# Optimization experiments

Measured on AMD Instinct MI355X. Metric: run time of the kernel, lower is better.

The kernel has to match this reference:

```python
import jax, jax.numpy as jnp
import numpy as np

LB_WEIGHT = 0.01  # load_balance_loss_weight


def setup_inputs() -> dict:
    key = jax.random.key(0)
    ks = jax.random.split(key, 5)
    B, S, D, F, E = 2, 2048, 1024, 4096, 8
    scale = 0.02
    return {
        "x": jax.random.normal(ks[0], (B, S, D), dtype=jnp.float32),
        "Wr": jax.random.normal(ks[1], (E, D), dtype=jnp.float32) * scale,
        "W1": jax.random.normal(ks[2], (E, F, D), dtype=jnp.float32) * scale,
        "b1": jnp.zeros((E, F), dtype=jnp.float32),
        "W2": jax.random.normal(ks[3], (E, D, F), dtype=jnp.float32) * scale,
        "b2": jnp.zeros((E, D), dtype=jnp.float32),
        "top_k": 2,
    }


def reference(x, Wr, W1, b1, W2, b2, top_k):
    B, S, D = x.shape
    E = Wr.shape[0]
    x_flat = x.reshape(-1, D)                      # (T, D)

    # Router: softmax over experts, then top-k with renormalized gates.
    router_logits = x_flat @ Wr.T                  # (T, E)
    router_probs = jax.nn.softmax(router_logits, axis=-1)
    topk_p, topk_idx = jax.lax.top_k(router_probs, top_k)   # (T, K)
    topk_p = topk_p / jnp.sum(topk_p, axis=-1, keepdims=True)

    # Combine weights per expert: w[t, e] = sum_k topk_p[t, k] * [idx[t, k] == e]
    one_hot = jax.nn.one_hot(topk_idx, E, dtype=x.dtype)     # (T, K, E)
    combine = jnp.einsum("tk,tke->te", topk_p, one_hot)      # (T, E)

    # Expert FFNs (dense over all experts; masked-out experts get zero weight).
    # FeedForward: Linear(D->F) -> GELU -> Linear(F->D); dropout is identity (eval).
    h = jnp.einsum("td,efd->tef", x_flat, W1) + b1           # (T, E, F)
    h = jax.nn.gelu(h)
    expert_out = jnp.einsum("tef,edf->ted", h, W2) + b2      # (T, E, D)

    out_flat = jnp.einsum("te,ted->td", combine, expert_out) # (T, D)
    output = out_flat.reshape(B, S, D)

    # Load-balance aux loss.
    expert_usage = jnp.mean(router_probs, axis=0)            # (E,)
    aux_loss = LB_WEIGHT * jnp.sum((expert_usage - 1.0 / E) ** 2)
    return output, aux_loss
```

## Files before the change

kernel.cpp:

```cpp
#include <hip/hip_runtime.h>
#include <hip/hip_bf16.h>
#include <stdint.h>

#define D_DIM 1024
#define F_DIM 4096
#define E_NUM 8
#define BM2 256
#define BN2 128
#define BK 64
#define MAXTILES 80
#define MAXT256 40

typedef __attribute__((ext_vector_type(4))) float f32x4;
typedef __attribute__((ext_vector_type(8))) short bf16x8;

#define C_CNT   0
#define C_CUR   8
#define C_OFF   16
#define C_NT    25
#define C_TE    26
#define C_TR    (26+MAXTILES)
#define C_USAGE (26+2*MAXTILES)

__device__ __forceinline__ void gload_lds16(const void* g, void* l) {
  __builtin_amdgcn_global_load_lds((const __attribute__((address_space(1))) void*)g,
                                   (__attribute__((address_space(3))) void*)l, 16, 0, 0);
}

__device__ __forceinline__ float bf2f(unsigned short u) {
  union { unsigned int i; float f; } c; c.i = ((unsigned int)u) << 16; return c.f;
}

__global__ void cvt_k(const float* __restrict__ s, unsigned short* __restrict__ d, int n4) {
  const int stride = gridDim.x * blockDim.x;
  for (int i = blockIdx.x * blockDim.x + threadIdx.x; i < n4; i += stride) {
    float4 v = ((const float4*)s)[i];
    __hip_bfloat16 h0 = __float2bfloat16(v.x);
    __hip_bfloat16 h1 = __float2bfloat16(v.y);
    __hip_bfloat16 h2 = __float2bfloat16(v.z);
    __hip_bfloat16 h3 = __float2bfloat16(v.w);
    ushort4 o;
    o.x = *(unsigned short*)&h0; o.y = *(unsigned short*)&h1;
    o.z = *(unsigned short*)&h2; o.w = *(unsigned short*)&h3;
    ((ushort4*)d)[i] = o;
  }
}

__global__ __launch_bounds__(256) void router_k(
    const float* __restrict__ x, const float* __restrict__ Wr,
    int* __restrict__ t2i, float* __restrict__ t2g,
    float* __restrict__ usage_part, unsigned short* __restrict__ xb, int T) {
  __shared__ float us[4][E_NUM];
  const int wave = threadIdx.x >> 6;
  const int lane = threadIdx.x & 63;
  const int gw = blockIdx.x * 4 + wave;
  const float4* xt = (const float4*)(x + (size_t)gw * D_DIM);
  const float4* wr4 = (const float4*)Wr;
  unsigned short* xrow = xb + (size_t)gw * D_DIM;
  float l[E_NUM] = {0.f,0.f,0.f,0.f,0.f,0.f,0.f,0.f};
#pragma unroll
  for (int it = 0; it < D_DIM / 256; it++) {
    const int i4 = it * 64 + lane;
    const float4 xv = xt[i4];
    __hip_bfloat16 c0 = __float2bfloat16(xv.x), c1 = __float2bfloat16(xv.y);
    __hip_bfloat16 c2 = __float2bfloat16(xv.z), c3 = __float2bfloat16(xv.w);
    ushort4 ov; ov.x = *(unsigned short*)&c0; ov.y = *(unsigned short*)&c1;
    ov.z = *(unsigned short*)&c2; ov.w = *(unsigned short*)&c3;
    ((ushort4*)xrow)[i4] = ov;
#pragma unroll
    for (int e = 0; e < E_NUM; e++) {
      const float4 w = wr4[e * (D_DIM / 4) + i4];
      l[e] += xv.x * w.x + xv.y * w.y + xv.z * w.z + xv.w * w.w;
    }
  }
#pragma unroll
  for (int e = 0; e < E_NUM; e++) {
    float v = l[e];
    v += __shfl_xor(v, 32); v += __shfl_xor(v, 16); v += __shfl_xor(v, 8);
    v += __shfl_xor(v, 4);  v += __shfl_xor(v, 2);  v += __shfl_xor(v, 1);
    l[e] = v;
  }
  float m = l[0];
#pragma unroll
  for (int e = 1; e < E_NUM; e++) m = fmaxf(m, l[e]);
  float p[E_NUM]; float s = 0.f;
#pragma unroll
  for (int e = 0; e < E_NUM; e++) { p[e] = expf(l[e] - m); s += p[e]; }
  const float inv = 1.0f / s;
  float v1 = l[0]; int i1 = 0;
#pragma unroll
  for (int e = 1; e < E_NUM; e++) { if (l[e] > v1) { v1 = l[e]; i1 = e; } }
  float v2 = -3.0e38f; int i2 = 0;
#pragma unroll
  for (int e = 0; e < E_NUM; e++) { if (e != i1 && l[e] > v2) { v2 = l[e]; i2 = e; } }
  const float p1 = expf(v1 - m);
  const float p2 = expf(v2 - m);
  const float gd = 1.0f / (p1 + p2);
  if (lane == 0) {
    t2i[gw * 2] = i1; t2i[gw * 2 + 1] = i2;
    t2g[gw * 2] = p1 * gd; t2g[gw * 2 + 1] = p2 * gd;
#pragma unroll
    for (int e = 0; e < E_NUM; e++) us[wave][e] = p[e] * inv;
  }
  __syncthreads();
  if (threadIdx.x < E_NUM) {
    const int e = threadIdx.x;
    usage_part[blockIdx.x * E_NUM + e] = us[0][e] + us[1][e] + us[2][e] + us[3][e];
  }
}

__global__ __launch_bounds__(256) void reduce_k(
    const float* __restrict__ usage_part, const int* __restrict__ t2i,
    int* __restrict__ ctrl, float* __restrict__ aux_out, int nblk, int T2, int T) {
  __shared__ float usum[E_NUM];
  __shared__ int hist[E_NUM];
  if (threadIdx.x < E_NUM) { usum[threadIdx.x] = 0.f; hist[threadIdx.x] = 0; }
  __syncthreads();
  {
    const int e = threadIdx.x & 7;
    const int chunk = threadIdx.x >> 3;
    float s = 0.f;
    for (int i = chunk; i < nblk; i += 32) s += usage_part[i * E_NUM + e];
    atomicAdd(&usum[e], s);
  }
  {
    int h[E_NUM] = {0,0,0,0,0,0,0,0};
    for (int i = threadIdx.x; i < T2; i += 256) h[t2i[i] & 7]++;
#pragma unroll
    for (int e = 0; e < E_NUM; e++) if (h[e]) atomicAdd(&hist[e], h[e]);
  }
  __syncthreads();
  if (threadIdx.x == 0) {
    int off = 0, nt = 0;
    float loss = 0.f;
    for (int e = 0; e < E_NUM; e++) {
      ctrl[C_CNT + e] = hist[e];
      ctrl[C_OFF + e] = off;
      ctrl[C_CUR + e] = off;
      const int c = hist[e];
      const int ntile = (c + BM2 - 1) / BM2;
      for (int i = 0; i < ntile; i++) {
        ctrl[C_TE + nt] = e;
        ctrl[C_TR + nt] = off + i * BM2;
        nt++;
      }
      off += c;
      const float um = usum[e] / (float)T - 1.0f / (float)E_NUM;
      loss += um * um;
    }
    ctrl[C_OFF + E_NUM] = off;
    ctrl[C_NT] = nt;
    aux_out[0] = 0.01f * loss;
  }
}

__global__ void scatter_k(const int* __restrict__ t2i, int* __restrict__ ctrl,
                          int* __restrict__ rmap, int* __restrict__ slots, int T) {
  const int t = blockIdx.x * blockDim.x + threadIdx.x;
  if (t >= T) return;
#pragma unroll
  for (int k = 0; k < 2; k++) {
    const int e = t2i[t * 2 + k];
    const int slot = atomicAdd(&ctrl[C_CUR + e], 1);
    rmap[slot] = t;
    slots[t * 2 + k] = slot;
  }
}

#define STAGE(K0, AL, BL)                                            \
  {                                                                  \
    _Pragma("unroll")                                                \
    for (int i = 0; i < 4; i++) gload_lds16(a_src[i] + (K0), AL[i]); \
    _Pragma("unroll")                                                \
    for (int j = 0; j < 2; j++) gload_lds16(b_src[j] + (K0), BL[j]); \
  }

#define COMPUTE(AC, BC)                                              \
  {                                                                  \
    _Pragma("unroll")                                                \
    for (int kh = 0; kh < 2; ++kh) {                                 \
      const int co = (((kh * 4 + ckq) ^ swz) << 4);                  \
      bf16x8 af[8], bfv[2];                                          \
      _Pragma("unroll")                                              \
      for (int mi = 0; mi < 8; mi++)                                 \
        af[mi] = *(const bf16x8*)((AC) + (rA + mi * 16) * 128 + co); \
      _Pragma("unroll")                                              \
      for (int ni = 0; ni < 2; ni++)                                 \
        bfv[ni] = *(const bf16x8*)((BC) + (rB + ni * 16) * 128 + co);\
      _Pragma("unroll")                                              \
      for (int mi = 0; mi < 8; mi++)                                 \
        _Pragma("unroll")                                            \
        for (int ni = 0; ni < 2; ni++)                               \
          acc[mi][ni] = __builtin_amdgcn_mfma_f32_16x16x32_bf16(af[mi], bfv[ni], acc[mi][ni], 0, 0, 0); \
    }                                                                \
  }

__global__ __launch_bounds__(512, 2) void gemm1_k(
    const unsigned short* __restrict__ xb, const unsigned short* __restrict__ W1b,
    const float* __restrict__ b1, unsigned short* __restrict__ hb,
    const int* __restrict__ rmap, const int* __restrict__ ctrl, int T2) {
  extern __shared__ char smem[];
  const int lin = blockIdx.x;
  const int lin2 = (lin & 7) * 160 + (lin >> 3);
  const int tile = lin2 >> 5;
  const int fbase = (lin2 & 31) * BN2;

  const int nt = ctrl[C_NT];
  if (tile >= nt) return;
  const int e = ctrl[C_TE + tile];
  const int rowbase = ctrl[C_TR + tile];
  const int row_end = ctrl[C_OFF + e + 1];

  const int tid = threadIdx.x;
  const int lane = tid & 63;
  const int wave = tid >> 6;

  const unsigned short* a_src[4];
  const unsigned short* b_src[2];
  char *aL0[4], *aL1[4], *bL0[2], *bL1[2];
#pragma unroll
  for (int i = 0; i < 4; i++) {
    const int c = tid + 512 * i;
    const int r = c >> 3, cc = c & 7;
    const int sc = cc ^ (r & 7);
    int pos = rowbase + r; pos = pos < T2 ? pos : T2 - 1;
    a_src[i] = xb + (size_t)rmap[pos] * D_DIM + sc * 8;
    aL0[i] = smem + c * 16;
    aL1[i] = smem + 32768 + c * 16;
  }
#pragma unroll
  for (int j = 0; j < 2; j++) {
    const int c2 = tid + 512 * j;
    const int r = c2 >> 3, cc = c2 & 7;
    const int sc = cc ^ (r & 7);
    b_src[j] = W1b + ((size_t)e * F_DIM + (size_t)(fbase + r)) * D_DIM + sc * 8;
    bL0[j] = smem + 65536 + c2 * 16;
    bL1[j] = smem + 81920 + c2 * 16;
  }
  const char* As0 = smem;          const char* As1 = smem + 32768;
  const char* Bs0 = smem + 65536;  const char* Bs1 = smem + 81920;

  f32x4 acc[8][2] = {};
  const int wm = wave >> 2, wn = wave & 3;
  const int rA = wm * 128 + (lane & 15);
  const int rB = wn * 32 + (lane & 15);
  const int swz = lane & 7;
  const int ckq = lane >> 4;

  STAGE(0, aL0, bL0);
  const int NK = D_DIM / BK;
  for (int kt = 0; kt < NK; kt += 2) {
    STAGE((kt + 1) * BK, aL1, bL1);
    asm volatile("s_waitcnt vmcnt(6)" ::: "memory");
    __builtin_amdgcn_s_barrier();
    __builtin_amdgcn_sched_barrier(0);
    COMPUTE(As0, Bs0);
    __builtin_amdgcn_sched_barrier(0);
    __builtin_amdgcn_s_barrier();
    if (kt + 2 < NK) {
      STAGE((kt + 2) * BK, aL0, bL0);
      asm volatile("s_waitcnt vmcnt(6)" ::: "memory");
    } else {
      asm volatile("s_waitcnt vmcnt(0)" ::: "memory");
    }
    __builtin_amdgcn_s_barrier();
    __builtin_amdgcn_sched_barrier(0);
    COMPUTE(As1, Bs1);
    __builtin_amdgcn_sched_barrier(0);
    __builtin_amdgcn_s_barrier();
  }

  const int r_rem = row_end - rowbase;
  const float* b1e = b1 + (size_t)e * F_DIM;
  float bias[2];
#pragma unroll
  for (int ni = 0; ni < 2; ni++)
    bias[ni] = b1e[fbase + wn * 32 + ni * 16 + (lane & 15)];
#pragma unroll
  for (int mi = 0; mi < 8; mi++) {
#pragma unroll
    for (int q = 0; q < 4; q++) {
      const int rr = wm * 128 + mi * 16 + (lane >> 4) * 4 + q;
      if (rr < r_rem) {
        unsigned short* hrow = hb + (size_t)(rowbase + rr) * F_DIM;
#pragma unroll
        for (int ni = 0; ni < 2; ni++) {
          const int col = fbase + wn * 32 + ni * 16 + (lane & 15);
          const float v = acc[mi][ni][q] + bias[ni];
          const float u2 = 1.5957691216057308f * (v + 0.044715f * v * v * v);
          const float gg = v / (1.0f + __expf(-u2));
          __hip_bfloat16 hv = __float2bfloat16(gg);
          hrow[col] = *(unsigned short*)&hv;
        }
      }
    }
  }
}

__global__ __launch_bounds__(512, 2) void gemm2_k(
    const unsigned short* __restrict__ hb, const unsigned short* __restrict__ W2b,
    unsigned short* __restrict__ y2, const int* __restrict__ ctrl, int T2) {
  extern __shared__ char smem[];
  const int lin = blockIdx.x;
  const int lin2 = (lin & 7) * 160 + (lin >> 3);
  const int tile = lin2 >> 5;
  const int rest = lin2 & 31;
  const int z = rest >> 3;
  const int dbase = (rest & 7) * BN2;

  const int nt = ctrl[C_NT];
  if (tile >= nt) return;
  const int e = ctrl[C_TE + tile];
  const int rowbase = ctrl[C_TR + tile];
  const int row_end = ctrl[C_OFF + e + 1];
  const int kt0 = z * (F_DIM / BK / 4);

  const int tid = threadIdx.x;
  const int lane = tid & 63;
  const int wave = tid >> 6;

  const unsigned short* a_src[4];
  const unsigned short* b_src[2];
  char *aL0[4], *aL1[4], *bL0[2], *bL1[2];
#pragma unroll
  for (int i = 0; i < 4; i++) {
    const int c = tid + 512 * i;
    const int r = c >> 3, cc = c & 7;
    const int sc = cc ^ (r & 7);
    int pos = rowbase + r; pos = pos < T2 ? pos : T2 - 1;
    a_src[i] = hb + (size_t)pos * F_DIM + sc * 8;
    aL0[i] = smem + c * 16;
    aL1[i] = smem + 32768 + c * 16;
  }
#pragma unroll
  for (int j = 0; j < 2; j++) {
    const int c2 = tid + 512 * j;
    const int r = c2 >> 3, cc = c2 & 7;
    const int sc = cc ^ (r & 7);
    b_src[j] = W2b + ((size_t)e * D_DIM + (size_t)(dbase + r)) * F_DIM + sc * 8;
    bL0[j] = smem + 65536 + c2 * 16;
    bL1[j] = smem + 81920 + c2 * 16;
  }
  const char* As0 = smem;          const char* As1 = smem + 32768;
  const char* Bs0 = smem + 65536;  const char* Bs1 = smem + 81920;

  f32x4 acc[8][2] = {};
  const int wm = wave >> 2, wn = wave & 3;
  const int rA = wm * 128 + (lane & 15);
  const int rB = wn * 32 + (lane & 15);
  const int swz = lane & 7;
  const int ckq = lane >> 4;

  const int NKH = F_DIM / BK / 4;
  STAGE(kt0 * BK, aL0, bL0);
  for (int kt = kt0; kt < kt0 + NKH; kt += 2) {
    STAGE((kt + 1) * BK, aL1, bL1);
    asm volatile("s_waitcnt vmcnt(6)" ::: "memory");
    __builtin_amdgcn_s_barrier();
    __builtin_amdgcn_sched_barrier(0);
    COMPUTE(As0, Bs0);
    __builtin_amdgcn_sched_barrier(0);
    __builtin_amdgcn_s_barrier();
    if (kt + 2 < kt0 + NKH) {
      STAGE((kt + 2) * BK, aL0, bL0);
      asm volatile("s_waitcnt vmcnt(6)" ::: "memory");
    } else {
      asm volatile("s_waitcnt vmcnt(0)" ::: "memory");
    }
    __builtin_amdgcn_s_barrier();
    __builtin_amdgcn_sched_barrier(0);
    COMPUTE(As1, Bs1);
    __builtin_amdgcn_sched_barrier(0);
    __builtin_amdgcn_s_barrier();
  }

  const int r_rem = row_end - rowbase;
  unsigned short* yz = y2 + (size_t)z * T2 * D_DIM;
#pragma unroll
  for (int mi = 0; mi < 8; mi++) {
#pragma unroll
    for (int q = 0; q < 4; q++) {
      const int rr = wm * 128 + mi * 16 + (lane >> 4) * 4 + q;
      if (rr < r_rem) {
        unsigned short* yrow = yz + (size_t)(rowbase + rr) * D_DIM;
#pragma unroll
        for (int ni = 0; ni < 2; ni++) {
          const int col = dbase + wn * 32 + ni * 16 + (lane & 15);
          __hip_bfloat16 hv = __float2bfloat16(acc[mi][ni][q]);
          yrow[col] = *(unsigned short*)&hv;
        }
      }
    }
  }
}

__global__ __launch_bounds__(256) void combine_k(
    const unsigned short* __restrict__ y2, const float* __restrict__ b2,
    const int* __restrict__ t2i, const float* __restrict__ t2g,
    const int* __restrict__ slots, float* __restrict__ out, int T2) {
  const int t = blockIdx.x;
  const int c4 = threadIdx.x;
  const int s0 = slots[t * 2], s1 = slots[t * 2 + 1];
  const int e0 = t2i[t * 2], e1 = t2i[t * 2 + 1];
  const float g0 = t2g[t * 2], g1 = t2g[t * 2 + 1];
  const size_t sl = (size_t)T2 * D_DIM;
  float sum0[4] = {0.f,0.f,0.f,0.f}, sum1[4] = {0.f,0.f,0.f,0.f};
#pragma unroll
  for (int zz = 0; zz < 4; zz++) {
    ushort4 a = ((const ushort4*)(y2 + zz * sl + (size_t)s0 * D_DIM))[c4];
    ushort4 b = ((const ushort4*)(y2 + zz * sl + (size_t)s1 * D_DIM))[c4];
    sum0[0] += bf2f(a.x); sum0[1] += bf2f(a.y); sum0[2] += bf2f(a.z); sum0[3] += bf2f(a.w);
    sum1[0] += bf2f(b.x); sum1[1] += bf2f(b.y); sum1[2] += bf2f(b.z); sum1[3] += bf2f(b.w);
  }
  float4 bb0 = ((const float4*)(b2 + (size_t)e0 * D_DIM))[c4];
  float4 bb1 = ((const float4*)(b2 + (size_t)e1 * D_DIM))[c4];
  float4 o;
  o.x = g0 * (sum0[0] + bb0.x) + g1 * (sum1[0] + bb1.x);
  o.y = g0 * (sum0[1] + bb0.y) + g1 * (sum1[1] + bb1.y);
  o.z = g0 * (sum0[2] + bb0.z) + g1 * (sum1[2] + bb1.z);
  o.w = g0 * (sum0[3] + bb0.w) + g1 * (sum1[3] + bb1.w);
  ((float4*)(out + (size_t)t * D_DIM))[c4] = o;
}

extern "C" void kernel_launch(void* const* d_in, const int* in_sizes, int n_in,
                              void* d_out, int out_size, void* d_ws, size_t ws_size,
                              hipStream_t stream) {
  const float* x  = (const float*)d_in[0];
  const float* Wr = (const float*)d_in[1];
  const float* W1 = (const float*)d_in[2];
  const float* b1 = (const float*)d_in[3];
  const float* W2 = (const float*)d_in[4];
  const float* b2 = (const float*)d_in[5];
  float* out = (float*)d_out;

  const int T = in_sizes[0] / D_DIM;
  const int T2 = T * 2;
  const int nblk = T / 4;

  char* ws = (char*)d_ws;
  size_t o = 0;
  unsigned short* xb  = (unsigned short*)(ws + o); o += (size_t)T * D_DIM * 2;
  unsigned short* W1b = (unsigned short*)(ws + o); o += (size_t)E_NUM * F_DIM * D_DIM * 2;
  unsigned short* W2b = (unsigned short*)(ws + o); o += (size_t)E_NUM * D_DIM * F_DIM * 2;
  unsigned short* hb  = (unsigned short*)(ws + o); o += (size_t)T2 * F_DIM * 2;
  int*   ctrl  = (int*)(ws + o);   o += 4096;
  int*   t2i   = (int*)(ws + o);   o += (size_t)T2 * 4;
  float* t2g   = (float*)(ws + o); o += (size_t)T2 * 4;
  int*   rmap  = (int*)(ws + o);   o += (size_t)T2 * 4;
  int*   slots = (int*)(ws + o);   o += (size_t)T2 * 4;
  float* usage_part = (float*)(ws + o); o += (size_t)nblk * E_NUM * 4;
  unsigned short* y2 = W1b;

  hipFuncSetAttribute((const void*)gemm1_k, hipFuncAttributeMaxDynamicSharedMemorySize, 98304);
  hipFuncSetAttribute((const void*)gemm2_k, hipFuncAttributeMaxDynamicSharedMemorySize, 98304);

  hipMemsetAsync(ctrl, 0, 4096, stream);

  cvt_k<<<1024, 256, 0, stream>>>(W1, W1b, E_NUM * F_DIM * D_DIM / 4);
  cvt_k<<<1024, 256, 0, stream>>>(W2, W2b, E_NUM * D_DIM * F_DIM / 4);

  router_k<<<nblk, 256, 0, stream>>>(x, Wr, t2i, t2g, usage_part, xb, T);
  reduce_k<<<1, 256, 0, stream>>>(usage_part, t2i, ctrl, out + (size_t)(out_size - 1), nblk, T2, T);
  scatter_k<<<(T + 255) / 256, 256, 0, stream>>>(t2i, ctrl, rmap, slots, T);

  gemm1_k<<<MAXT256 * 32, 512, 98304, stream>>>(xb, W1b, b1, hb, rmap, ctrl, T2);
  gemm2_k<<<MAXT256 * 32, 512, 98304, stream>>>(hb, W2b, y2, ctrl, T2);
  combine_k<<<T, 256, 0, stream>>>(y2, b2, t2i, t2g, slots, out, T2);
}
```

Measured before the change: 377.3 us.

## Replace double-buffered LDS pipeline with single-buffer load-then-compute in expert GEMMs

Both expert GEMM kernels drop the two-stage LDS ping-pong, where the next K tile was prefetched while the current one was computed. Each iteration now loads one tile, waits for all loads to finish, computes, then barriers. LDS per block drops from 96KB to 48KB, which could let more blocks share a CU. In exchange, global-load latency is no longer hidden behind MFMA work within a block.

```diff
diff --git a/kernel.cpp b/kernel.cpp
--- a/kernel.cpp
+++ b/kernel.cpp
@@ -167,12 +167,13 @@
   }
 }
 
-#define STAGE(K0, AL, BL)                                            \
+
+#define STAGE(K0)                                                    \
   {                                                                  \
     _Pragma("unroll")                                                \
-    for (int i = 0; i < 4; i++) gload_lds16(a_src[i] + (K0), AL[i]); \
+    for (int i = 0; i < 4; i++) gload_lds16(a_src[i] + (K0), aL[i]); \
     _Pragma("unroll")                                                \
-    for (int j = 0; j < 2; j++) gload_lds16(b_src[j] + (K0), BL[j]); \
+    for (int j = 0; j < 2; j++) gload_lds16(b_src[j] + (K0), bL[j]); \
   }
 
 #define COMPUTE(AC, BC)                                              \
@@ -217,7 +218,7 @@
 
   const unsigned short* a_src[4];
   const unsigned short* b_src[2];
-  char *aL0[4], *aL1[4], *bL0[2], *bL1[2];
+  char *aL[4], *bL[2];
 #pragma unroll
   for (int i = 0; i < 4; i++) {
     const int c = tid + 512 * i;
@@ -225,8 +226,7 @@
     const int sc = cc ^ (r & 7);
     int pos = rowbase + r; pos = pos < T2 ? pos : T2 - 1;
     a_src[i] = xb + (size_t)rmap[pos] * D_DIM + sc * 8;
-    aL0[i] = smem + c * 16;
-    aL1[i] = smem + 32768 + c * 16;
+    aL[i] = smem + c * 16;
   }
 #pragma unroll
   for (int j = 0; j < 2; j++) {
@@ -234,11 +234,10 @@
     const int r = c2 >> 3, cc = c2 & 7;
     const int sc = cc ^ (r & 7);
     b_src[j] = W1b + ((size_t)e * F_DIM + (size_t)(fbase + r)) * D_DIM + sc * 8;
-    bL0[j] = smem + 65536 + c2 * 16;
-    bL1[j] = smem + 81920 + c2 * 16;
-  }
-  const char* As0 = smem;          const char* As1 = smem + 32768;
-  const char* Bs0 = smem + 65536;  const char* Bs1 = smem + 81920;
+    bL[j] = smem + 32768 + c2 * 16;
+  }
+  const char* As = smem;
+  const char* Bs = smem + 32768;
 
   f32x4 acc[8][2] = {};
   const int wm = wave >> 2, wn = wave & 3;
@@ -247,25 +246,13 @@
   const int swz = lane & 7;
   const int ckq = lane >> 4;
 
-  STAGE(0, aL0, bL0);
   const int NK = D_DIM / BK;
-  for (int kt = 0; kt < NK; kt += 2) {
-    STAGE((kt + 1) * BK, aL1, bL1);
-    asm volatile("s_waitcnt vmcnt(6)" ::: "memory");
+  for (int kt = 0; kt < NK; ++kt) {
+    STAGE(kt * BK);
+    asm volatile("s_waitcnt vmcnt(0)" ::: "memory");
     __builtin_amdgcn_s_barrier();
     __builtin_amdgcn_sched_barrier(0);
-    COMPUTE(As0, Bs0);
-    __builtin_amdgcn_sched_barrier(0);
-    __builtin_amdgcn_s_barrier();
-    if (kt + 2 < NK) {
-      STAGE((kt + 2) * BK, aL0, bL0);
-      asm volatile("s_waitcnt vmcnt(6)" ::: "memory");
-    } else {
-      asm volatile("s_waitcnt vmcnt(0)" ::: "memory");
-    }
-    __builtin_amdgcn_s_barrier();
-    __builtin_amdgcn_sched_barrier(0);
-    COMPUTE(As1, Bs1);
+    COMPUTE(As, Bs);
     __builtin_amdgcn_sched_barrier(0);
     __builtin_amdgcn_s_barrier();
   }
@@ -321,7 +308,7 @@
 
   const unsigned short* a_src[4];
   const unsigned short* b_src[2];
-  char *aL0[4], *aL1[4], *bL0[2], *bL1[2];
+  char *aL[4], *bL[2];
 #pragma unroll
   for (int i = 0; i < 4; i++) {
     const int c = tid + 512 * i;
@@ -329,8 +316,7 @@
     const int sc = cc ^ (r & 7);
     int pos = rowbase + r; pos = pos < T2 ? pos : T2 - 1;
     a_src[i] = hb + (size_t)pos * F_DIM + sc * 8;
-    aL0[i] = smem + c * 16;
-    aL1[i] = smem + 32768 + c * 16;
+    aL[i] = smem + c * 16;
   }
 #pragma unroll
   for (int j = 0; j < 2; j++) {
@@ -338,11 +324,10 @@
     const int r = c2 >> 3, cc = c2 & 7;
     const int sc = cc ^ (r & 7);
     b_src[j] = W2b + ((size_t)e * D_DIM + (size_t)(dbase + r)) * F_DIM + sc * 8;
-    bL0[j] = smem + 65536 + c2 * 16;
-    bL1[j] = smem + 81920 + c2 * 16;
-  }
-  const char* As0 = smem;          const char* As1 = smem + 32768;
-  const char* Bs0 = smem + 65536;  const char* Bs1 = smem + 81920;
+    bL[j] = smem + 32768 + c2 * 16;
+  }
+  const char* As = smem;
+  const char* Bs = smem + 32768;
 
   f32x4 acc[8][2] = {};
   const int wm = wave >> 2, wn = wave & 3;
@@ -352,24 +337,12 @@
   const int ckq = lane >> 4;
 
   const int NKH = F_DIM / BK / 4;
-  STAGE(kt0 * BK, aL0, bL0);
-  for (int kt = kt0; kt < kt0 + NKH; kt += 2) {
-    STAGE((kt + 1) * BK, aL1, bL1);
-    asm volatile("s_waitcnt vmcnt(6)" ::: "memory");
+  for (int kt = kt0; kt < kt0 + NKH; ++kt) {
+    STAGE(kt * BK);
+    asm volatile("s_waitcnt vmcnt(0)" ::: "memory");
     __builtin_amdgcn_s_barrier();
     __builtin_amdgcn_sched_barrier(0);
-    COMPUTE(As0, Bs0);
-    __builtin_amdgcn_sched_barrier(0);
-    __builtin_amdgcn_s_barrier();
-    if (kt + 2 < kt0 + NKH) {
-      STAGE((kt + 2) * BK, aL0, bL0);
-      asm volatile("s_waitcnt vmcnt(6)" ::: "memory");
-    } else {
-      asm volatile("s_waitcnt vmcnt(0)" ::: "memory");
-    }
-    __builtin_amdgcn_s_barrier();
-    __builtin_amdgcn_sched_barrier(0);
-    COMPUTE(As1, Bs1);
+    COMPUTE(As, Bs);
     __builtin_amdgcn_sched_barrier(0);
     __builtin_amdgcn_s_barrier();
   }
@@ -451,8 +424,8 @@
   float* usage_part = (float*)(ws + o); o += (size_t)nblk * E_NUM * 4;
   unsigned short* y2 = W1b;
 
-  hipFuncSetAttribute((const void*)gemm1_k, hipFuncAttributeMaxDynamicSharedMemorySize, 98304);
-  hipFuncSetAttribute((const void*)gemm2_k, hipFuncAttributeMaxDynamicSharedMemorySize, 98304);
+  hipFuncSetAttribute((const void*)gemm1_k, hipFuncAttributeMaxDynamicSharedMemorySize, 49152);
+  hipFuncSetAttribute((const void*)gemm2_k, hipFuncAttributeMaxDynamicSharedMemorySize, 49152);
 
   hipMemsetAsync(ctrl, 0, 4096, stream);
 
@@ -463,7 +436,7 @@
   reduce_k<<<1, 256, 0, stream>>>(usage_part, t2i, ctrl, out + (size_t)(out_size - 1), nblk, T2, T);
   scatter_k<<<(T + 255) / 256, 256, 0, stream>>>(t2i, ctrl, rmap, slots, T);
 
-  gemm1_k<<<MAXT256 * 32, 512, 98304, stream>>>(xb, W1b, b1, hb, rmap, ctrl, T2);
-  gemm2_k<<<MAXT256 * 32, 512, 98304, stream>>>(hb, W2b, y2, ctrl, T2);
+  gemm1_k<<<MAXT256 * 32, 512, 49152, stream>>>(xb, W1b, b1, hb, rmap, ctrl, T2);
+  gemm2_k<<<MAXT256 * 32, 512, 49152, stream>>>(hb, W2b, y2, ctrl, T2);
   combine_k<<<T, 256, 0, stream>>>(y2, b2, t2i, t2g, slots, out, T2);
 }
```

After: 360.9 us, median of 3. 4.3% less time.
